# Optimization experiments

Hardware: AMD Instinct MI355X
Metric: run time of the kernel (lower is better)

Reference implementation:

```python
import jax, jax.numpy as jnp
import numpy as np

EPS = 1e-06


def setup_inputs() -> dict:
    key = jax.random.key(0)
    k1, k2 = jax.random.split(key)
    N, M, D = 8192, 8192, 512
    first_vector = jax.random.normal(k1, (N, D), dtype=jnp.float32)
    second_vector = jax.random.normal(k2, (M, D), dtype=jnp.float32)
    return {"first_vector": first_vector, "second_vector": second_vector, "normalize": 1}


def reference(first_vector, second_vector, normalize):
    # Pairwise dot products: [N, M]. Mathematically identical to the
    # broadcast multiply + sum over D in the torch module, but as a GEMM.
    sim = jnp.einsum('nd,md->nm', first_vector, second_vector)
    if normalize:
        # Note: module divides by sqrt(|a| * |b|) + eps (geometric mean of
        # norms, not the product) -- reproduce exactly.
        n1 = jnp.linalg.norm(first_vector, axis=1)[:, None]   # [N, 1]
        n2 = jnp.linalg.norm(second_vector, axis=1)[None, :]  # [1, M]
        sim = sim / (jnp.sqrt(n1 * n2) + EPS)
    return sim
```

## Files before the change

kernel.cpp:

```cpp
#include <hip/hip_runtime.h>
#include <hip/hip_bf16.h>
#include <math.h>

#define EPS 1e-6f

constexpr int D  = 512;
constexpr int BM = 128;
constexpr int BN = 128;

typedef __attribute__((ext_vector_type(8))) short  short8;
typedef __attribute__((ext_vector_type(4))) float  floatx4;

__device__ inline unsigned short f2bf(float f) {
  union { __hip_bfloat16 h; unsigned short u; } cvt;
  cvt.h = __float2bfloat16(f);
  return cvt.u;
}

__global__ __launch_bounds__(256) void prep_kernel(
    const float* __restrict__ src, __hip_bfloat16* __restrict__ dst,
    float* __restrict__ isn, int nrows) {
  const int lane = threadIdx.x & 63;
  const int row  = blockIdx.x * 4 + (threadIdx.x >> 6);
  if (row >= nrows) return;

  const float4* p4 = (const float4*)(src + (size_t)row * D);
  const float4 v1 = p4[lane];
  const float4 v2 = p4[lane + 64];

  if (dst != nullptr) {
    ushort4 u1, u2;
    u1.x = f2bf(v1.x); u1.y = f2bf(v1.y); u1.z = f2bf(v1.z); u1.w = f2bf(v1.w);
    u2.x = f2bf(v2.x); u2.y = f2bf(v2.y); u2.z = f2bf(v2.z); u2.w = f2bf(v2.w);
    ushort4* drow = (ushort4*)(dst + (size_t)row * D);
    drow[lane]      = u1;
    drow[lane + 64] = u2;
  }

  float ss = v1.x * v1.x + v1.y * v1.y + v1.z * v1.z + v1.w * v1.w
           + v2.x * v2.x + v2.y * v2.y + v2.z * v2.z + v2.w * v2.w;
  #pragma unroll
  for (int o = 32; o > 0; o >>= 1) ss += __shfl_down(ss, o);
  if (lane == 0) {
    const float n1 = sqrtf(ss);
    isn[row] = 1.0f / sqrtf(n1);
  }
}

__global__ __launch_bounds__(256) void gemm_bt_kernel(
    const __hip_bfloat16* __restrict__ A, const __hip_bfloat16* __restrict__ B,
    const float* __restrict__ ia, const float* __restrict__ ib,
    const int* __restrict__ nrmflag, float* __restrict__ C,
    int N, int M) {
  __shared__ __align__(16) __hip_bfloat16 sA[2][BM * 32];
  __shared__ __align__(16) __hip_bfloat16 sB[2][BN * 32];

  const int t    = threadIdx.x;
  const int w    = t >> 6;
  const int lane = t & 63;
  const int wm   = w & 1;
  const int wn   = w >> 1;

  const size_t rowA0 = (size_t)blockIdx.x * BM;
  const size_t rowB0 = (size_t)blockIdx.y * BN;

  floatx4 acc[4][4];
  #pragma unroll
  for (int i = 0; i < 4; ++i)
    #pragma unroll
    for (int j = 0; j < 4; ++j) acc[i][j] = (floatx4){0.f, 0.f, 0.f, 0.f};

  const int ldRow = lane >> 2;
  const int ldCol = (lane & 3) * 8;
  const int fr = lane & 15;
  const int fq = (lane >> 4) * 8;

  const __hip_bfloat16* gA0 = A + (rowA0 + (size_t)ldRow) * D + ldCol;
  const __hip_bfloat16* gB0 = B + (rowB0 + (size_t)ldRow) * D + ldCol;

  for (int k0 = 0; k0 < D; k0 += 64) {
    #pragma unroll
    for (int h = 0; h < 2; ++h) {
      const int kc = k0 + h * 32;
      #pragma unroll
      for (int j = 0; j < 2; ++j) {
        const int c = w * 2 + j;
        __builtin_amdgcn_global_load_lds(
            (const __attribute__((address_space(1))) void*)(gA0 + (size_t)(c * 16) * D + kc),
            (__attribute__((address_space(3))) void*)(&sA[h][c * 512]), 16, 0, 0);
        __builtin_amdgcn_global_load_lds(
            (const __attribute__((address_space(1))) void*)(gB0 + (size_t)(c * 16) * D + kc),
            (__attribute__((address_space(3))) void*)(&sB[h][c * 512]), 16, 0, 0);
      }
    }
    __syncthreads();

    #pragma unroll
    for (int h = 0; h < 2; ++h) {
      short8 af[4], bf[4];
      #pragma unroll
      for (int i = 0; i < 4; ++i) {
        af[i] = *(const short8*)(&sA[h][(wm * 64 + i * 16 + fr) * 32 + fq]);
        bf[i] = *(const short8*)(&sB[h][(wn * 64 + i * 16 + fr) * 32 + fq]);
      }
      #pragma unroll
      for (int i = 0; i < 4; ++i)
        #pragma unroll
        for (int j = 0; j < 4; ++j)
          acc[i][j] = __builtin_amdgcn_mfma_f32_16x16x32_bf16(af[i], bf[j], acc[i][j], 0, 0, 0);
    }
    __syncthreads();
  }

  const int nrm = *nrmflag;
  const int cq  = lane >> 4;
  const int cc  = lane & 15;

  float ibv[4];
  #pragma unroll
  for (int j = 0; j < 4; ++j)
    ibv[j] = nrm ? ib[rowB0 + wn * 64 + j * 16 + cc] : 1.0f;

  #pragma unroll
  for (int i = 0; i < 4; ++i) {
    const size_t rbase = rowA0 + wm * 64 + i * 16 + cq * 4;
    float4 iav4 = nrm ? *(const float4*)(ia + rbase) : (float4){1.f, 1.f, 1.f, 1.f};
    const float iavr[4] = {iav4.x, iav4.y, iav4.z, iav4.w};
    #pragma unroll
    for (int r = 0; r < 4; ++r) {
      const size_t row = rbase + r;
      float* crow = C + row * (size_t)M + rowB0 + wn * 64 + cc;
      #pragma unroll
      for (int j = 0; j < 4; ++j)
        crow[j * 16] = acc[i][j][r] * iavr[r] * ibv[j];
    }
  }
}

__global__ __launch_bounds__(256) void fb_gemm(
    const float* __restrict__ A, const float* __restrict__ B,
    const float* __restrict__ ia, const float* __restrict__ ib,
    const int* __restrict__ nrmflag, float* __restrict__ C, int N, int M) {
  __shared__ float sA[32][33];
  __shared__ float sB[32][33];
  const int tx = threadIdx.x & 31;
  const int ty = threadIdx.x >> 5;
  const size_t row0 = (size_t)blockIdx.y * 32;
  const size_t col0 = (size_t)blockIdx.x * 32;
  float acc[4] = {0.f, 0.f, 0.f, 0.f};
  for (int k0 = 0; k0 < D; k0 += 32) {
    #pragma unroll
    for (int r = 0; r < 4; ++r) {
      sA[ty + 8 * r][tx] = A[(row0 + ty + 8 * r) * D + k0 + tx];
      sB[ty + 8 * r][tx] = B[(col0 + ty + 8 * r) * D + k0 + tx];
    }
    __syncthreads();
    #pragma unroll 8
    for (int kk = 0; kk < 32; ++kk) {
      const float bv = sB[tx][kk];
      #pragma unroll
      for (int r = 0; r < 4; ++r) acc[r] += sA[ty + 8 * r][kk] * bv;
    }
    __syncthreads();
  }
  const int nrm  = *nrmflag;
  const float iv = ib[col0 + tx];
  #pragma unroll
  for (int r = 0; r < 4; ++r) {
    const size_t row = row0 + ty + 8 * r;
    float v = acc[r];
    if (nrm) {
      const float denom = 1.0f / (ia[row] * iv) + EPS;
      v /= denom;
    }
    C[row * (size_t)M + col0 + tx] = v;
  }
}

extern "C" void kernel_launch(void* const* d_in, const int* in_sizes, int n_in,
                              void* d_out, int out_size, void* d_ws, size_t ws_size,
                              hipStream_t stream) {
  const float* A   = (const float*)d_in[0];
  const float* B   = (const float*)d_in[1];
  const int*   nrm = (const int*)d_in[2];
  float*       C   = (float*)d_out;
  const int N = in_sizes[0] / D;
  const int M = in_sizes[1] / D;

  float* iaN = (float*)d_ws;
  float* ibN = iaN + N;
  __hip_bfloat16* Abf = (__hip_bfloat16*)(ibN + M);
  __hip_bfloat16* Bbf = Abf + (size_t)N * D;

  const size_t need = (size_t)(N + M) * sizeof(float)
                    + (size_t)(N + M) * D * sizeof(__hip_bfloat16);
  const bool fast = (ws_size >= need) && (N % BM == 0) && (M % BN == 0);

  prep_kernel<<<(N + 3) / 4, 256, 0, stream>>>(A, fast ? Abf : nullptr, iaN, N);
  prep_kernel<<<(M + 3) / 4, 256, 0, stream>>>(B, fast ? Bbf : nullptr, ibN, M);

  if (fast) {
    gemm_bt_kernel<<<dim3(N / BM, M / BN), 256, 0, stream>>>(Abf, Bbf, iaN, ibN, nrm, C, N, M);
  } else {
    fb_gemm<<<dim3(M / 32, N / 32), 256, 0, stream>>>(A, B, iaN, ibN, nrm, C, N, M);
  }
}
```

Measured before the change: 350.9 us.

## Replace 128x128 GEMM with 256x256 tile, 8-wave, double-buffered swizzled LDS pipeline

Rewrites the bf16 MFMA GEMM to use 256x256 output tiles with 512 threads, an XOR-swizzled LDS layout, and double-buffered K tiles whose global loads overlap with MFMA work through explicit vmcnt waits and barriers. It also remaps block IDs across groups of eight to improve L2 locality and raises MFMA wave priority with setprio. The aim is higher data reuse per loaded tile and less exposed load latency. In exchange it uses 128KB of LDS and many accumulator registers, which limits occupancy, and relies on hand-tuned wait counts that must match the number of outstanding loads.

After: 370.8 us. 5.7% more time.

```diff
diff --git a/kernel.cpp b/kernel.cpp
--- a/kernel.cpp
+++ b/kernel.cpp
@@ -5,8 +5,8 @@
 #define EPS 1e-6f
 
 constexpr int D  = 512;
-constexpr int BM = 128;
-constexpr int BN = 128;
+constexpr int BM = 256;
+constexpr int BN = 256;
 
 typedef __attribute__((ext_vector_type(8))) short  short8;
 typedef __attribute__((ext_vector_type(4))) float  floatx4;
@@ -47,69 +47,148 @@
   }
 }
 
-__global__ __launch_bounds__(256) void gemm_bt_kernel(
+
+#define GLD(srcp, ldsoff_shorts)                                              \
+  __builtin_amdgcn_global_load_lds(                                           \
+      (const __attribute__((address_space(1))) void*)(srcp),                  \
+      (__attribute__((address_space(3))) void*)(smem + (ldsoff_shorts)),      \
+      16, 0, 0)
+
+#define STAGE_HALF(gbase, lbase)                                              \
+  do {                                                                        \
+    GLD((gbase) + soff,                   (lbase) + t * 8);                   \
+    GLD((gbase) + soff + (size_t)64 * D,  (lbase) + (t + 512) * 8);           \
+  } while (0)
+
+#define STAGE_KTILE(kt, b)                                                    \
+  do {                                                                        \
+    STAGE_HALF(gA + (kt) * 64,                   ((b) * 2 + 0) * 8192);       \
+    STAGE_HALF(gA + (kt) * 64 + (size_t)128 * D, ((b) * 2 + 1) * 8192);       \
+    STAGE_HALF(gB + (kt) * 64,                   32768 + ((b) * 2 + 0) * 8192); \
+    STAGE_HALF(gB + (kt) * 64 + (size_t)128 * D, 32768 + ((b) * 2 + 1) * 8192); \
+  } while (0)
+
+#define RD(p, m, off) (*(const short8*)((p) + (m) * 2048 + rbyte + (off)))
+
+#define MM2(mi, ni)                                                           \
+  do {                                                                        \
+    acc[mi][ni] = __builtin_amdgcn_mfma_f32_16x16x32_bf16(                    \
+        aR[(mi) & 3][0], bR[ni][0], acc[mi][ni], 0, 0, 0);                    \
+    acc[mi][ni] = __builtin_amdgcn_mfma_f32_16x16x32_bf16(                    \
+        aR[(mi) & 3][1], bR[ni][1], acc[mi][ni], 0, 0, 0);                    \
+  } while (0)
+
+#define BAR   __builtin_amdgcn_s_barrier()
+#define LGKM0 do { asm volatile("s_waitcnt lgkmcnt(0)" ::: "memory");         \
+                   __builtin_amdgcn_sched_barrier(0); } while (0)
+#define VM8   asm volatile("s_waitcnt vmcnt(8)" ::: "memory")
+#define VM0   asm volatile("s_waitcnt vmcnt(0)" ::: "memory")
+#define NOOP  do {} while (0)
+
+#define KTILE(b, STAGE_STMT, WAITV)                                           \
+  do {                                                                        \
+    const char* pA_ = (const char*)smem + ((b) * 2 + wm) * 16384;             \
+    const char* pB_ = (const char*)smem + 65536                               \
+                      + ((b) * 2 + (wn >> 1)) * 16384 + (wn & 1) * 8192;      \
+                                 \
+    aR[0][0] = RD(pA_, 0, off0); aR[0][1] = RD(pA_, 0, off1);                 \
+    aR[1][0] = RD(pA_, 1, off0); aR[1][1] = RD(pA_, 1, off1);                 \
+    aR[2][0] = RD(pA_, 2, off0); aR[2][1] = RD(pA_, 2, off1);                 \
+    aR[3][0] = RD(pA_, 3, off0); aR[3][1] = RD(pA_, 3, off1);                 \
+    bR[0][0] = RD(pB_, 0, off0); bR[0][1] = RD(pB_, 0, off1);                 \
+    bR[1][0] = RD(pB_, 1, off0); bR[1][1] = RD(pB_, 1, off1);                 \
+    BAR; LGKM0;                                                               \
+    __builtin_amdgcn_s_setprio(1);                                            \
+    MM2(0,0); MM2(1,0); MM2(2,0); MM2(3,0);                                   \
+    MM2(0,1); MM2(1,1); MM2(2,1); MM2(3,1);                                   \
+    __builtin_amdgcn_s_setprio(0);                                            \
+    BAR;                                                                      \
+                                                              \
+    bR[2][0] = RD(pB_, 2, off0); bR[2][1] = RD(pB_, 2, off1);                 \
+    bR[3][0] = RD(pB_, 3, off0); bR[3][1] = RD(pB_, 3, off1);                 \
+    BAR; LGKM0;                                                               \
+    __builtin_amdgcn_s_setprio(1);                                            \
+    MM2(0,2); MM2(1,2); MM2(2,2); MM2(3,2);                                   \
+    MM2(0,3); MM2(1,3); MM2(2,3); MM2(3,3);                                   \
+    __builtin_amdgcn_s_setprio(0);                                            \
+    BAR;                                                                      \
+                                               \
+    aR[0][0] = RD(pA_, 4, off0); aR[0][1] = RD(pA_, 4, off1);                 \
+    aR[1][0] = RD(pA_, 5, off0); aR[1][1] = RD(pA_, 5, off1);                 \
+    aR[2][0] = RD(pA_, 6, off0); aR[2][1] = RD(pA_, 6, off1);                 \
+    aR[3][0] = RD(pA_, 7, off0); aR[3][1] = RD(pA_, 7, off1);                 \
+    BAR; LGKM0;                                                               \
+    __builtin_amdgcn_s_setprio(1);                                            \
+    MM2(4,2); MM2(5,2); MM2(6,2); MM2(7,2);                                   \
+    MM2(4,3); MM2(5,3); MM2(6,3); MM2(7,3);                                   \
+    __builtin_amdgcn_s_setprio(0);                                            \
+    BAR;                                                                      \
+       \
+    STAGE_STMT;                                                               \
+    BAR;                                                                      \
+    __builtin_amdgcn_s_setprio(1);                                            \
+    MM2(4,0); MM2(5,0); MM2(6,0); MM2(7,0);                                   \
+    MM2(4,1); MM2(5,1); MM2(6,1); MM2(7,1);                                   \
+    __builtin_amdgcn_s_setprio(0);                                            \
+    WAITV;                                                                    \
+    BAR;                                                                      \
+  } while (0)
+
+__global__ __launch_bounds__(512, 2) void gemm256_kernel(
     const __hip_bfloat16* __restrict__ A, const __hip_bfloat16* __restrict__ B,
     const float* __restrict__ ia, const float* __restrict__ ib,
     const int* __restrict__ nrmflag, float* __restrict__ C,
     int N, int M) {
-  __shared__ __align__(16) __hip_bfloat16 sA[2][BM * 32];
-  __shared__ __align__(16) __hip_bfloat16 sB[2][BN * 32];
+  __shared__ __align__(128) short smem[65536];
 
   const int t    = threadIdx.x;
+  const int lane = t & 63;
   const int w    = t >> 6;
-  const int lane = t & 63;
-  const int wm   = w & 1;
-  const int wn   = w >> 1;
-
-  const size_t rowA0 = (size_t)blockIdx.x * BM;
-  const size_t rowB0 = (size_t)blockIdx.y * BN;
-
-  floatx4 acc[4][4];
-  #pragma unroll
-  for (int i = 0; i < 4; ++i)
+  const int wm   = w >> 2;
+  const int wn   = w & 3;
+
+  int bid = blockIdx.y * gridDim.x + blockIdx.x;
+  const int nwg = (int)(gridDim.x * gridDim.y);
+  if ((nwg & 7) == 0) bid = (bid & 7) * (nwg >> 3) + (bid >> 3);
+  const int ix = bid % (int)gridDim.x;
+  const int iy = bid / (int)gridDim.x;
+  const size_t rowA0 = (size_t)ix * BM;
+  const size_t rowB0 = (size_t)iy * BN;
+
+  const int srow  = t >> 3;
+  const int sslot = (t & 7) ^ (srow & 7);
+  const size_t soff = (size_t)srow * D + sslot * 8;
+  const unsigned short* gA = (const unsigned short*)A + rowA0 * D;
+  const unsigned short* gB = (const unsigned short*)B + rowB0 * D;
+
+  const int fr    = lane & 15;
+  const int g4    = lane >> 4;
+  const int rbyte = fr * 128;
+  const int off0  = ((g4    ) ^ (fr & 7)) * 16;
+  const int off1  = ((g4 + 4) ^ (fr & 7)) * 16;
+
+  floatx4 acc[8][4];
+  #pragma unroll
+  for (int i = 0; i < 8; ++i)
     #pragma unroll
     for (int j = 0; j < 4; ++j) acc[i][j] = (floatx4){0.f, 0.f, 0.f, 0.f};
 
-  const int ldRow = lane >> 2;
-  const int ldCol = (lane & 3) * 8;
-  const int fr = lane & 15;
-  const int fq = (lane >> 4) * 8;
-
-  const __hip_bfloat16* gA0 = A + (rowA0 + (size_t)ldRow) * D + ldCol;
-  const __hip_bfloat16* gB0 = B + (rowB0 + (size_t)ldRow) * D + ldCol;
-
-  for (int k0 = 0; k0 < D; k0 += 64) {
-    #pragma unroll
-    for (int h = 0; h < 2; ++h) {
-      const int kc = k0 + h * 32;
-      #pragma unroll
-      for (int j = 0; j < 2; ++j) {
-        const int c = w * 2 + j;
-        __builtin_amdgcn_global_load_lds(
-            (const __attribute__((address_space(1))) void*)(gA0 + (size_t)(c * 16) * D + kc),
-            (__attribute__((address_space(3))) void*)(&sA[h][c * 512]), 16, 0, 0);
-        __builtin_amdgcn_global_load_lds(
-            (const __attribute__((address_space(1))) void*)(gB0 + (size_t)(c * 16) * D + kc),
-            (__attribute__((address_space(3))) void*)(&sB[h][c * 512]), 16, 0, 0);
-      }
-    }
-    __syncthreads();
-
-    #pragma unroll
-    for (int h = 0; h < 2; ++h) {
-      short8 af[4], bf[4];
-      #pragma unroll
-      for (int i = 0; i < 4; ++i) {
-        af[i] = *(const short8*)(&sA[h][(wm * 64 + i * 16 + fr) * 32 + fq]);
-        bf[i] = *(const short8*)(&sB[h][(wn * 64 + i * 16 + fr) * 32 + fq]);
-      }
-      #pragma unroll
-      for (int i = 0; i < 4; ++i)
-        #pragma unroll
-        for (int j = 0; j < 4; ++j)
-          acc[i][j] = __builtin_amdgcn_mfma_f32_16x16x32_bf16(af[i], bf[j], acc[i][j], 0, 0, 0);
-    }
-    __syncthreads();
+  short8 aR[4][2], bR[4][2];
+
+  STAGE_KTILE(0, 0);
+  STAGE_KTILE(1, 1);
+  VM8;
+  BAR;
+
+  #pragma unroll
+  for (int it = 0; it < 4; ++it) {
+    if (it < 3) {
+      KTILE(0, STAGE_KTILE(it * 2 + 2, 0), VM8);
+      KTILE(1, STAGE_KTILE(it * 2 + 3, 1), VM8);
+    } else {
+      KTILE(0, NOOP, VM0);
+      KTILE(1, NOOP, NOOP);
+    }
   }
 
   const int nrm = *nrmflag;
@@ -118,21 +197,20 @@
 
   float ibv[4];
   #pragma unroll
-  for (int j = 0; j < 4; ++j)
-    ibv[j] = nrm ? ib[rowB0 + wn * 64 + j * 16 + cc] : 1.0f;
-
-  #pragma unroll
-  for (int i = 0; i < 4; ++i) {
-    const size_t rbase = rowA0 + wm * 64 + i * 16 + cq * 4;
+  for (int n = 0; n < 4; ++n)
+    ibv[n] = nrm ? ib[rowB0 + wn * 64 + n * 16 + cc] : 1.0f;
+
+  #pragma unroll
+  for (int m = 0; m < 8; ++m) {
+    const size_t rbase = rowA0 + wm * 128 + m * 16 + cq * 4;
     float4 iav4 = nrm ? *(const float4*)(ia + rbase) : (float4){1.f, 1.f, 1.f, 1.f};
     const float iavr[4] = {iav4.x, iav4.y, iav4.z, iav4.w};
     #pragma unroll
     for (int r = 0; r < 4; ++r) {
-      const size_t row = rbase + r;
-      float* crow = C + row * (size_t)M + rowB0 + wn * 64 + cc;
+      float* crow = C + (rbase + r) * (size_t)M + rowB0 + wn * 64 + cc;
       #pragma unroll
-      for (int j = 0; j < 4; ++j)
-        crow[j * 16] = acc[i][j][r] * iavr[r] * ibv[j];
+      for (int n = 0; n < 4; ++n)
+        crow[n * 16] = acc[m][n][r] * iavr[r] * ibv[n];
     }
   }
 }
@@ -200,7 +278,7 @@
   prep_kernel<<<(M + 3) / 4, 256, 0, stream>>>(B, fast ? Bbf : nullptr, ibN, M);
 
   if (fast) {
-    gemm_bt_kernel<<<dim3(N / BM, M / BN), 256, 0, stream>>>(Abf, Bbf, iaN, ibN, nrm, C, N, M);
+    gemm256_kernel<<<dim3(N / BM, M / BN), 512, 0, stream>>>(Abf, Bbf, iaN, ibN, nrm, C, N, M);
   } else {
     fb_gemm<<<dim3(M / 32, N / 32), 256, 0, stream>>>(A, B, iaN, ibN, nrm, C, N, M);
   }
```

## Fold normalization into bf16 inputs, remap blocks per XCD, use nontemporal stores

Applied to the files above, without the earlier changes.

The inverse fourth-root-norm scale is now applied to each row before the bf16 conversion in the prep kernel, so the GEMM epilogue no longer loads scale vectors or multiplies. The GEMM block index is remapped so each of the 8 XCDs works on a contiguous band of A row tiles, aiming for better L2 reuse. Output stores become nontemporal to avoid polluting cache with the 256MB result. Scaling before rounding changes bf16 rounding slightly and drops the EPS term, as the old fast path also did.

New measurement: 338.3 us. -3.6%, faster.

```diff
diff --git a/kernel.cpp b/kernel.cpp
--- a/kernel.cpp
+++ b/kernel.cpp
@@ -19,7 +19,7 @@
 
 __global__ __launch_bounds__(256) void prep_kernel(
     const float* __restrict__ src, __hip_bfloat16* __restrict__ dst,
-    float* __restrict__ isn, int nrows) {
+    float* __restrict__ isn, const int* __restrict__ nrmflag, int nrows) {
   const int lane = threadIdx.x & 63;
   const int row  = blockIdx.x * 4 + (threadIdx.x >> 6);
   if (row >= nrows) return;
@@ -28,30 +28,30 @@
   const float4 v1 = p4[lane];
   const float4 v2 = p4[lane + 64];
 
+  float ss = v1.x * v1.x + v1.y * v1.y + v1.z * v1.z + v1.w * v1.w
+           + v2.x * v2.x + v2.y * v2.y + v2.z * v2.z + v2.w * v2.w;
+  #pragma unroll
+  for (int o = 32; o > 0; o >>= 1) ss += __shfl_xor(ss, o);
+
+  const float s4 = rsqrtf(sqrtf(ss));
+  if (lane == 0) isn[row] = s4;
+
   if (dst != nullptr) {
+    const float s = (*nrmflag) ? s4 : 1.0f;
     ushort4 u1, u2;
-    u1.x = f2bf(v1.x); u1.y = f2bf(v1.y); u1.z = f2bf(v1.z); u1.w = f2bf(v1.w);
-    u2.x = f2bf(v2.x); u2.y = f2bf(v2.y); u2.z = f2bf(v2.z); u2.w = f2bf(v2.w);
+    u1.x = f2bf(v1.x * s); u1.y = f2bf(v1.y * s);
+    u1.z = f2bf(v1.z * s); u1.w = f2bf(v1.w * s);
+    u2.x = f2bf(v2.x * s); u2.y = f2bf(v2.y * s);
+    u2.z = f2bf(v2.z * s); u2.w = f2bf(v2.w * s);
     ushort4* drow = (ushort4*)(dst + (size_t)row * D);
     drow[lane]      = u1;
     drow[lane + 64] = u2;
   }
-
-  float ss = v1.x * v1.x + v1.y * v1.y + v1.z * v1.z + v1.w * v1.w
-           + v2.x * v2.x + v2.y * v2.y + v2.z * v2.z + v2.w * v2.w;
-  #pragma unroll
-  for (int o = 32; o > 0; o >>= 1) ss += __shfl_down(ss, o);
-  if (lane == 0) {
-    const float n1 = sqrtf(ss);
-    isn[row] = 1.0f / sqrtf(n1);
-  }
 }
 
 __global__ __launch_bounds__(256) void gemm_bt_kernel(
     const __hip_bfloat16* __restrict__ A, const __hip_bfloat16* __restrict__ B,
-    const float* __restrict__ ia, const float* __restrict__ ib,
-    const int* __restrict__ nrmflag, float* __restrict__ C,
-    int N, int M) {
+    float* __restrict__ C, int N, int M) {
   __shared__ __align__(16) __hip_bfloat16 sA[2][BM * 32];
   __shared__ __align__(16) __hip_bfloat16 sB[2][BN * 32];
 
@@ -61,8 +61,23 @@
   const int wm   = w & 1;
   const int wn   = w >> 1;
 
-  const size_t rowA0 = (size_t)blockIdx.x * BM;
-  const size_t rowB0 = (size_t)blockIdx.y * BN;
+  size_t rowA0, rowB0;
+  {
+    const int gx   = (int)gridDim.x;
+    const int orig = (int)(blockIdx.y * gridDim.x + blockIdx.x);
+    if ((gx & 7) == 0) {
+      const int bandw = gx >> 3;
+      const int xcd = orig & 7;
+      const int loc = orig >> 3;
+      const int ir  = xcd * bandw + (loc % bandw);
+      const int ic  = loc / bandw;
+      rowA0 = (size_t)ir * BM;
+      rowB0 = (size_t)ic * BN;
+    } else {
+      rowA0 = (size_t)blockIdx.x * BM;
+      rowB0 = (size_t)blockIdx.y * BN;
+    }
+  }
 
   floatx4 acc[4][4];
   #pragma unroll
@@ -112,27 +127,18 @@
     __syncthreads();
   }
 
-  const int nrm = *nrmflag;
-  const int cq  = lane >> 4;
-  const int cc  = lane & 15;
-
-  float ibv[4];
-  #pragma unroll
-  for (int j = 0; j < 4; ++j)
-    ibv[j] = nrm ? ib[rowB0 + wn * 64 + j * 16 + cc] : 1.0f;
+  const int cq = lane >> 4;
+  const int cc = lane & 15;
 
   #pragma unroll
   for (int i = 0; i < 4; ++i) {
     const size_t rbase = rowA0 + wm * 64 + i * 16 + cq * 4;
-    float4 iav4 = nrm ? *(const float4*)(ia + rbase) : (float4){1.f, 1.f, 1.f, 1.f};
-    const float iavr[4] = {iav4.x, iav4.y, iav4.z, iav4.w};
     #pragma unroll
     for (int r = 0; r < 4; ++r) {
-      const size_t row = rbase + r;
-      float* crow = C + row * (size_t)M + rowB0 + wn * 64 + cc;
+      float* crow = C + (rbase + r) * (size_t)M + rowB0 + wn * 64 + cc;
       #pragma unroll
       for (int j = 0; j < 4; ++j)
-        crow[j * 16] = acc[i][j][r] * iavr[r] * ibv[j];
+        __builtin_nontemporal_store(acc[i][j][r], crow + j * 16);
     }
   }
 }
@@ -196,11 +202,11 @@
                     + (size_t)(N + M) * D * sizeof(__hip_bfloat16);
   const bool fast = (ws_size >= need) && (N % BM == 0) && (M % BN == 0);
 
-  prep_kernel<<<(N + 3) / 4, 256, 0, stream>>>(A, fast ? Abf : nullptr, iaN, N);
-  prep_kernel<<<(M + 3) / 4, 256, 0, stream>>>(B, fast ? Bbf : nullptr, ibN, M);
+  prep_kernel<<<(N + 3) / 4, 256, 0, stream>>>(A, fast ? Abf : nullptr, iaN, nrm, N);
+  prep_kernel<<<(M + 3) / 4, 256, 0, stream>>>(B, fast ? Bbf : nullptr, ibN, nrm, M);
 
   if (fast) {
-    gemm_bt_kernel<<<dim3(N / BM, M / BN), 256, 0, stream>>>(Abf, Bbf, iaN, ibN, nrm, C, N, M);
+    gemm_bt_kernel<<<dim3(N / BM, M / BN), 256, 0, stream>>>(Abf, Bbf, C, N, M);
   } else {
     fb_gemm<<<dim3(M / 32, N / 32), 256, 0, stream>>>(A, B, iaN, ibN, nrm, C, N, M);
   }
```
